# Optimization experiments

Measured on AMD Instinct MI355X. Metric: run time of the kernel, lower is better.

Reference implementation:

```python
import jax, jax.numpy as jnp
import numpy as np

VOCAB = 50257
SEQ = 2048
EMB = 512
BATCH = 8


def setup_inputs() -> dict:
    key = jax.random.key(0)
    k1, k2, k3 = jax.random.split(key, 3)
    tokens = jax.random.randint(k1, (BATCH, SEQ), 0, VOCAB, dtype=jnp.int64 if jax.config.jax_enable_x64 else jnp.int32)
    W_emb = jax.random.normal(k2, (EMB, VOCAB), dtype=jnp.float32)
    W_pos = jax.random.normal(k3, (SEQ, EMB), dtype=jnp.float32)
    return {"tokens": tokens, "W_emb": W_emb, "W_pos": W_pos}


def reference(tokens, W_emb, W_pos):
    # Original: one_hot(tokens, V).float() @ W_emb.T  -> identical to gathering
    # columns of W_emb, i.e. rows of W_emb.T. Shapes: (B,S) -> (B,S,E)
    tok_emb = jnp.take(W_emb.T, tokens, axis=0)  # (B, S, E)
    # positional weight (S, E) broadcasts over batch
    return tok_emb + W_pos
```

## Files before the change

### kernel.cpp

```cpp
#include <hip/hip_runtime.h>

#define VOCAB 50257
#define SEQ   2048
#define EMB   512
#define BATCH 8
#define NTOK  (BATCH * SEQ)

typedef float floatx2 __attribute__((ext_vector_type(2)));


#define HEAD_OFF 0
#define NEXT_OFF 50432
#define WS_INTS  (NEXT_OFF + NTOK)

__global__ __launch_bounds__(256)
void init_head_k(int* __restrict__ head) {
    const int i = blockIdx.x * 256 + threadIdx.x;
    if (i < VOCAB) head[i] = -1;
}

__global__ __launch_bounds__(256)
void links_k(const int* __restrict__ tokens, int* __restrict__ head,
             int* __restrict__ next) {
    const int i = blockIdx.x * 256 + threadIdx.x;
    next[i] = atomicExch(&head[tokens[i]], i);
}

__global__ __launch_bounds__(256)
void slab_scatter_k(const int* __restrict__ head,
                    const int* __restrict__ next,
                    const float* __restrict__ W,
                    const floatx2* __restrict__ Wpos2,
                    floatx2* __restrict__ out2) {
    __shared__ float slab[64][129];
    __shared__ int   u_vl[64];
    __shared__ int   u_hd[64];
    __shared__ int   nused_s;

    const int v0   = blockIdx.x * 64;
    const int eoff = blockIdx.y * 128;
    const int tid  = threadIdx.x;
    const int lane = tid & 63;
    const int wv   = tid >> 6;
    const int v    = v0 + lane;

    if (tid < 64) {
        const int h = (v < VOCAB) ? head[v] : -1;
        const unsigned long long m = __ballot(h >= 0);
        const int pos = __popcll(m & ((1ull << lane) - 1ull));
        if (h >= 0) { u_vl[pos] = lane; u_hd[pos] = h; }
        if (lane == 0) nused_s = (int)__popcll(m);
    }

    if (v < VOCAB) {
        const float* rp = W + (size_t)(eoff + wv) * VOCAB + v;
        const int cbase = (wv & 1) * 64 + (wv >> 1);
#pragma unroll
        for (int j = 0; j < 32; ++j) {
            slab[lane][cbase + 2 * j] = rp[(size_t)(4 * j) * VOCAB];
        }
    }
    __syncthreads();

    const int nused = nused_s;
    const int ecol2 = (eoff >> 1) + lane;
    for (int u = wv; u < nused; u += 4) {
        const int vl = u_vl[u];
        int p = u_hd[u];
        floatx2 col;
        col.x = slab[vl][lane];
        col.y = slab[vl][64 + lane];
        while (p >= 0) {
            const int s = p & (SEQ - 1);
            const floatx2 r = col + Wpos2[(size_t)s * (EMB / 2) + ecol2];
            __builtin_nontemporal_store(
                r, &out2[(size_t)p * (EMB / 2) + ecol2]);
            p = next[p];
        }
    }
}

typedef float floatx4 __attribute__((ext_vector_type(4)));
__global__ __launch_bounds__(256)
void gather_direct_k(const int* __restrict__ tokens,
                     const float* __restrict__ W_emb,
                     const floatx4* __restrict__ Wpos,
                     floatx4* __restrict__ out) {
    const int idx = blockIdx.x * blockDim.x + threadIdx.x;
    const int e4  = idx & (EMB / 4 - 1);
    const int ts  = idx >> 7;
    const int s   = ts & (SEQ - 1);
    const int t   = tokens[ts];
    const size_t base = (size_t)(4 * e4) * VOCAB + (size_t)t;
    floatx4 r;
    r.x = W_emb[base];
    r.y = W_emb[base + (size_t)VOCAB];
    r.z = W_emb[base + (size_t)(2 * VOCAB)];
    r.w = W_emb[base + (size_t)(3 * VOCAB)];
    __builtin_nontemporal_store(r + Wpos[(size_t)s * (EMB / 4) + e4], &out[idx]);
}

extern "C" void kernel_launch(void* const* d_in, const int* in_sizes, int n_in,
                              void* d_out, int out_size, void* d_ws, size_t ws_size,
                              hipStream_t stream) {
    const int*   tokens = (const int*)d_in[0];
    const float* W_emb  = (const float*)d_in[1];
    const float* W_pos  = (const float*)d_in[2];
    float*       out    = (float*)d_out;

    const size_t need = (size_t)WS_INTS * sizeof(int);
    if (ws_size >= need) {
        int* head = (int*)d_ws + HEAD_OFF;
        int* next = (int*)d_ws + NEXT_OFF;

        init_head_k<<<(VOCAB + 255) / 256, 256, 0, stream>>>(head);
        links_k<<<NTOK / 256, 256, 0, stream>>>(tokens, head, next);
        slab_scatter_k<<<dim3((VOCAB + 63) / 64, EMB / 128), 256, 0, stream>>>(
            head, next, W_emb, (const floatx2*)W_pos, (floatx2*)out);
    } else {
        const int gblocks = BATCH * SEQ * (EMB / 4) / 256;
        gather_direct_k<<<gblocks, 256, 0, stream>>>(tokens, W_emb,
                                                     (const floatx4*)W_pos,
                                                     (floatx4*)out);
    }
}
```

Before: 177.1 us.

## Retile slab scatter to wide vocab tiles with vectorized aligned W_emb loads

Changes the slab tile from 64 vocab by 128 embedding to 256 vocab by 32 embedding, and loads each W_emb row with 16-byte vector loads realigned by a per-row shift into LDS. The used-token compaction now spans all four waves, and each half-wave scatters one token column as 128-byte float stores. The aim is to stream the whole embedding table with wider, coalesced reads and keep more blocks resident (launch_bounds 4). In exchange, each scattered row is now written in narrower 32-float chunks, and the vector loads over-read at unaligned row starts.

```diff
diff --git a/kernel.cpp b/kernel.cpp
--- a/kernel.cpp
+++ b/kernel.cpp
@@ -6,12 +6,17 @@
 #define BATCH 8
 #define NTOK  (BATCH * SEQ)
 
-typedef float floatx2 __attribute__((ext_vector_type(2)));
+typedef float floatx4 __attribute__((ext_vector_type(4)));
 
 
 #define HEAD_OFF 0
 #define NEXT_OFF 50432
 #define WS_INTS  (NEXT_OFF + NTOK)
+
+#define VTILE 256
+#define ETILE 32
+#define NBX   197
+#define SLDS  257
 
 __global__ __launch_bounds__(256)
 void init_head_k(int* __restrict__ head) {
@@ -26,61 +31,85 @@
     next[i] = atomicExch(&head[tokens[i]], i);
 }
 
-__global__ __launch_bounds__(256)
+__global__ __launch_bounds__(256, 4)
 void slab_scatter_k(const int* __restrict__ head,
                     const int* __restrict__ next,
                     const float* __restrict__ W,
-                    const floatx2* __restrict__ Wpos2,
-                    floatx2* __restrict__ out2) {
-    __shared__ float slab[64][129];
-    __shared__ int   u_vl[64];
-    __shared__ int   u_hd[64];
-    __shared__ int   nused_s;
+                    const float* __restrict__ Wpos,
+                    float* __restrict__ out) {
+    __shared__ float slab[ETILE][SLDS];
+    __shared__ int   u_vl[VTILE];
+    __shared__ int   u_hd[VTILE];
+    __shared__ int   wcnt[4];
 
-    const int v0   = blockIdx.x * 64;
-    const int eoff = blockIdx.y * 128;
+    const int bx   = blockIdx.x;
+    const int v0   = bx * VTILE;
+    const int e0   = blockIdx.y * ETILE;
     const int tid  = threadIdx.x;
     const int lane = tid & 63;
     const int wv   = tid >> 6;
-    const int v    = v0 + lane;
 
-    if (tid < 64) {
-        const int h = (v < VOCAB) ? head[v] : -1;
-        const unsigned long long m = __ballot(h >= 0);
-        const int pos = __popcll(m & ((1ull << lane) - 1ull));
-        if (h >= 0) { u_vl[pos] = lane; u_hd[pos] = h; }
-        if (lane == 0) nused_s = (int)__popcll(m);
-    }
+    const int vme = v0 + wv * 64 + lane;
+    const int h   = (vme < VOCAB) ? head[vme] : -1;
+    const unsigned long long m = __ballot(h >= 0);
+    const int pos = (int)__popcll(m & ((1ull << lane) - 1ull));
+    if (lane == 0) wcnt[wv] = (int)__popcll(m);
 
-    if (v < VOCAB) {
-        const float* rp = W + (size_t)(eoff + wv) * VOCAB + v;
-        const int cbase = (wv & 1) * 64 + (wv >> 1);
+    if (bx != NBX - 1) {
 #pragma unroll
-        for (int j = 0; j < 32; ++j) {
-            slab[lane][cbase + 2 * j] = rp[(size_t)(4 * j) * VOCAB];
+        for (int r8 = 0; r8 < 8; ++r8) {
+            const int r = r8 * 4 + wv;
+            const int e = e0 + r;
+            const size_t A = (size_t)e * VOCAB + v0;
+            const int shift = e & 3;
+            const floatx4 x =
+                *(reinterpret_cast<const floatx4*>(W + (A - shift)) + lane);
+            const int c0 = 4 * lane - shift;
+#pragma unroll
+            for (int i = 0; i < 4; ++i)
+                if (c0 + i >= 0) slab[r][c0 + i] = x[i];
+            if (lane < shift)
+                slab[r][VTILE - shift + lane] = W[A + VTILE - shift + lane];
+        }
+    } else {
+#pragma unroll
+        for (int r8 = 0; r8 < 8; ++r8) {
+            const int r = r8 * 4 + wv;
+            const size_t A = (size_t)(e0 + r) * VOCAB + v0;
+#pragma unroll
+            for (int j = 0; j < 4; ++j) {
+                const int c = 64 * j + lane;
+                if (v0 + c < VOCAB) slab[r][c] = W[A + c];
+            }
         }
     }
     __syncthreads();
 
-    const int nused = nused_s;
-    const int ecol2 = (eoff >> 1) + lane;
-    for (int u = wv; u < nused; u += 4) {
+    int off = 0;
+#pragma unroll
+    for (int w = 0; w < 4; ++w)
+        if (w < wv) off += wcnt[w];
+    if (h >= 0) { u_vl[off + pos] = wv * 64 + lane; u_hd[off + pos] = h; }
+    const int nused = wcnt[0] + wcnt[1] + wcnt[2] + wcnt[3];
+    __syncthreads();
+
+    const int half = lane >> 5;
+    const int l32  = lane & 31;
+    const float* wp = Wpos + e0 + l32;
+    float*       op = out  + e0 + l32;
+    for (int u = 2 * wv + half; u < nused; u += 8) {
         const int vl = u_vl[u];
         int p = u_hd[u];
-        floatx2 col;
-        col.x = slab[vl][lane];
-        col.y = slab[vl][64 + lane];
+        const float col = slab[l32][vl];
         while (p >= 0) {
             const int s = p & (SEQ - 1);
-            const floatx2 r = col + Wpos2[(size_t)s * (EMB / 2) + ecol2];
-            __builtin_nontemporal_store(
-                r, &out2[(size_t)p * (EMB / 2) + ecol2]);
+            __builtin_nontemporal_store(col + wp[(size_t)s * EMB],
+                                        op + (size_t)p * EMB);
             p = next[p];
         }
     }
 }
 
-typedef float floatx4 __attribute__((ext_vector_type(4)));
 __global__ __launch_bounds__(256)
 void gather_direct_k(const int* __restrict__ tokens,
                      const float* __restrict__ W_emb,
@@ -115,8 +144,8 @@
 
         init_head_k<<<(VOCAB + 255) / 256, 256, 0, stream>>>(head);
         links_k<<<NTOK / 256, 256, 0, stream>>>(tokens, head, next);
-        slab_scatter_k<<<dim3((VOCAB + 63) / 64, EMB / 128), 256, 0, stream>>>(
-            head, next, W_emb, (const floatx2*)W_pos, (floatx2*)out);
+        slab_scatter_k<<<dim3(NBX, EMB / ETILE), 256, 0, stream>>>(
+            head, next, W_emb, W_pos, out);
     } else {
         const int gblocks = BATCH * SEQ * (EMB / 4) / 256;
         gather_direct_k<<<gblocks, 256, 0, stream>>>(tokens, W_emb,
```

Result: slower. 201.0 us (+13.5%).
